# Kernel optimization log

Measured on AMD Instinct MI355X. Metric: run time of the kernel, lower is better.

## Reference

```python
import jax, jax.numpy as jnp
import numpy as np

B, D = 8192, 1024

def setup_inputs() -> dict:
    key = jax.random.key(0)
    ks = jax.random.split(key, 5)
    scale = 1.0 / np.sqrt(D)
    return {
        "x": jax.random.normal(ks[0], (B, D), dtype=jnp.float32),
        "h": jax.random.normal(ks[1], (B, D), dtype=jnp.float32),
        "c": jax.random.normal(ks[2], (B, D), dtype=jnp.float32),
        # gate order: [input, forget, output, candidate]
        "Wx": jax.random.normal(ks[3], (4, D, D), dtype=jnp.float32) * scale,
        "Wh": jax.random.normal(ks[4], (4, D, D), dtype=jnp.float32) * scale,
    }

def reference(x, h, c, Wx, Wh):
    # two batched GEMMs covering all 8 projections: [B,D] x [4,D,D] -> [4,B,D]
    gx = jnp.einsum('bd,gdk->gbk', x, Wx)
    gh = jnp.einsum('bd,gdk->gbk', h, Wh)
    g = gx + gh
    i = jax.nn.sigmoid(g[0])
    f = jax.nn.sigmoid(g[1])
    o = jax.nn.sigmoid(g[2])
    u = jnp.tanh(g[3])
    c_t = i * u + f * c
    h_t = o * jnp.tanh(c_t)
    return (h_t, c_t)
```

## Files before the change

kernel.cpp:

```cpp
#include <hip/hip_runtime.h>
#include <hip/hip_bf16.h>
#include <cstdint>


#define B_DIM 8192
#define D_DIM 1024
#define K_DIM 2048

typedef __attribute__((ext_vector_type(8))) short bf16x8;
typedef __attribute__((ext_vector_type(4))) float f32x4;
typedef __attribute__((ext_vector_type(4))) unsigned int u32x4;

static __device__ __forceinline__ unsigned short f2bf(float f) {
  union { float f; unsigned int u; } v; v.f = f;
  unsigned int u = v.u;
  unsigned int r = (u + 0x7FFFu + ((u >> 16) & 1u)) >> 16;
  return (unsigned short)r;
}

static __device__ __forceinline__ void load16(const void* gp, void* lp) {
  __builtin_amdgcn_global_load_lds(
      (const __attribute__((address_space(1))) void*)gp,
      (__attribute__((address_space(3))) void*)lp, 16, 0, 0);
}

static __device__ __forceinline__ float sigmoid_f(float x) {
  return 1.0f / (1.0f + __expf(-x));
}
static __device__ __forceinline__ float tanh_f(float x) {
  float e = __expf(-2.0f * fabsf(x));
  float r = (1.0f - e) / (1.0f + e);
  return copysignf(r, x);
}

__global__ __launch_bounds__(256) void pack_a_kernel(
    const float* __restrict__ x, const float* __restrict__ h,
    unsigned short* __restrict__ Apack) {
  int t = blockIdx.x * 256 + threadIdx.x;
  size_t base = (size_t)t * 8;
  int b = (int)(base >> 11);
  int k = (int)(base & 2047);
  const float* src = (k < 1024) ? (x + (size_t)b * 1024 + k)
                                : (h + (size_t)b * 1024 + (k - 1024));
  float4 v0 = ((const float4*)src)[0];
  float4 v1 = ((const float4*)src)[1];
  union { unsigned short s[8]; u32x4 v; } o;
  o.s[0] = f2bf(v0.x); o.s[1] = f2bf(v0.y); o.s[2] = f2bf(v0.z); o.s[3] = f2bf(v0.w);
  o.s[4] = f2bf(v1.x); o.s[5] = f2bf(v1.y); o.s[6] = f2bf(v1.z); o.s[7] = f2bf(v1.w);
  *(u32x4*)(Apack + base) = o.v;
}

__global__ __launch_bounds__(256) void prep_w_kernel(
    const float* __restrict__ Wx, const float* __restrict__ Wh,
    unsigned short* __restrict__ Wt) {
  __shared__ float tile[32][33];
  int bid = blockIdx.x;
  int g = bid >> 11;
  int rem = bid & 2047;
  int kt = rem >> 5;
  int nt = rem & 31;
  int k0 = kt * 32, n0 = nt * 32;
  int tx = threadIdx.x & 31, ty = threadIdx.x >> 5;
  const float* Wsrc;
  int ks;
  if (k0 < 1024) { Wsrc = Wx + (size_t)g * 1048576; ks = k0; }
  else           { Wsrc = Wh + (size_t)g * 1048576; ks = k0 - 1024; }
  #pragma unroll
  for (int s = 0; s < 4; ++s) {
    int r = ty + s * 8;
    tile[r][tx] = Wsrc[(size_t)(ks + r) * 1024 + n0 + tx];
  }
  __syncthreads();
  #pragma unroll
  for (int s = 0; s < 4; ++s) {
    int r = ty + s * 8;
    Wt[(size_t)((g << 10) + n0 + r) * 2048 + k0 + tx] = f2bf(tile[tx][r]);
  }
}

__global__ __launch_bounds__(256, 2) void lstm_gemm_kernel(
    const unsigned short* __restrict__ Apack,
    const unsigned short* __restrict__ Wt,
    const float* __restrict__ cprev,
    float* __restrict__ out) {
  extern __shared__ char lds[];
  const int tid = threadIdx.x;
  const int l = tid & 63;
  const int w = tid >> 6;
  const int bid = blockIdx.x;
  const int mt = bid >> 5;
  const int nt = bid & 31;
  const int m0 = mt << 7;
  const int n0 = nt << 5;

  f32x4 acc[4][2][2];
  #pragma unroll
  for (int g = 0; g < 4; ++g)
    #pragma unroll
    for (int a = 0; a < 2; ++a)
      #pragma unroll
      for (int b = 0; b < 2; ++b) acc[g][a][b] = (f32x4)0.0f;

  auto stage = [&](int buf, int t) {
    const int k0 = t << 6;
    char* base = lds + buf * 32768;
    #pragma unroll
    for (int j = 0; j < 4; ++j) {
      int c = j * 256 + tid;
      int Dd = c << 4;
      int row = Dd >> 7;
      int kbs = (Dd & 127) ^ ((row & 7) << 4);
      const unsigned short* gp = Apack + (size_t)(m0 + row) * 2048 + k0 + (kbs >> 1);
      load16(gp, base + ((c & ~63) << 4));
    }
    #pragma unroll
    for (int g = 0; g < 4; ++g) {
      int Dd = tid << 4;
      int row = Dd >> 7;
      int kbs = (Dd & 127) ^ ((row & 7) << 4);
      const unsigned short* gp =
          Wt + (size_t)((g << 10) + n0 + row) * 2048 + k0 + (kbs >> 1);
      load16(gp, base + 16384 + (g << 12) + ((tid & ~63) << 4));
    }
  };

  const int lr = l & 15;
  const int kgrp = (l >> 4) << 4;
  const int arow = w * 32 + lr;
  const int sA = (arow & 7) << 4;
  const int sB = (lr & 7) << 4;

  stage(0, 0);
  int cur = 0;
  for (int t = 0; t < 32; ++t) {
    __syncthreads();
    if (t + 1 < 32) stage(cur ^ 1, t + 1);
    const char* Ab = lds + cur * 32768;
    const char* Bb = Ab + 16384;
    #pragma unroll
    for (int ks = 0; ks < 2; ++ks) {
      const int kb = ks * 64 + kgrp;
      bf16x8 a0 = *(const bf16x8*)(Ab + arow * 128 + (kb ^ sA));
      bf16x8 a1 = *(const bf16x8*)(Ab + (arow + 16) * 128 + (kb ^ sA));
      #pragma unroll
      for (int g = 0; g < 4; ++g) {
        const char* Bg = Bb + (g << 12);
        bf16x8 b0 = *(const bf16x8*)(Bg + lr * 128 + (kb ^ sB));
        bf16x8 b1 = *(const bf16x8*)(Bg + (lr + 16) * 128 + (kb ^ sB));
        acc[g][0][0] = __builtin_amdgcn_mfma_f32_16x16x32_bf16(a0, b0, acc[g][0][0], 0, 0, 0);
        acc[g][0][1] = __builtin_amdgcn_mfma_f32_16x16x32_bf16(a0, b1, acc[g][0][1], 0, 0, 0);
        acc[g][1][0] = __builtin_amdgcn_mfma_f32_16x16x32_bf16(a1, b0, acc[g][1][0], 0, 0, 0);
        acc[g][1][1] = __builtin_amdgcn_mfma_f32_16x16x32_bf16(a1, b1, acc[g][1][1], 0, 0, 0);
      }
    }
    cur ^= 1;
  }

  const int rbase = m0 + w * 32;
  #pragma unroll
  for (int mf = 0; mf < 2; ++mf) {
    #pragma unroll
    for (int nf = 0; nf < 2; ++nf) {
      int col = n0 + nf * 16 + lr;
      #pragma unroll
      for (int j = 0; j < 4; ++j) {
        int rrow = rbase + mf * 16 + ((l >> 4) << 2) + j;
        float gi = acc[0][mf][nf][j];
        float gf = acc[1][mf][nf][j];
        float go = acc[2][mf][nf][j];
        float gu = acc[3][mf][nf][j];
        float i_ = sigmoid_f(gi);
        float f_ = sigmoid_f(gf);
        float o_ = sigmoid_f(go);
        float u_ = tanh_f(gu);
        size_t idx = (size_t)rrow * 1024 + col;
        float ct = i_ * u_ + f_ * cprev[idx];
        float ht = o_ * tanh_f(ct);
        out[idx] = ht;
        out[8388608 + idx] = ct;
      }
    }
  }
}

extern "C" void kernel_launch(void* const* d_in, const int* in_sizes, int n_in,
                              void* d_out, int out_size, void* d_ws, size_t ws_size,
                              hipStream_t stream) {
  const float* x  = (const float*)d_in[0];
  const float* h  = (const float*)d_in[1];
  const float* c  = (const float*)d_in[2];
  const float* Wx = (const float*)d_in[3];
  const float* Wh = (const float*)d_in[4];
  float* out = (float*)d_out;

  unsigned short* Apack = (unsigned short*)d_ws;
  unsigned short* Wt = (unsigned short*)((char*)d_ws + 33554432);

  pack_a_kernel<<<8192, 256, 0, stream>>>(x, h, Apack);
  prep_w_kernel<<<8192, 256, 0, stream>>>(Wx, Wh, Wt);
  lstm_gemm_kernel<<<2048, 256, 65536, stream>>>(Apack, Wt, c, out);
}
```

Baseline: 171.3 us.

## Enlarge GEMM tile to 128x64 with 8 waves and triple-buffered LDS pipeline

The fused LSTM GEMM now uses 512-thread blocks, each computing a 128-row by 64-column (times 4 gates) tile. Work is split over 8 waves in a 2x4 grid, and each wave holds 16 accumulator fragments, which gives more MFMA reuse per LDS load. The K loop switches from double buffering with a syncthreads per step to a three-slot ring that prefetches two stages ahead, using explicit vmcnt waits, raw barriers, sched_barrier fences and setprio around the MFMA bursts. The block needs 144 KB of dynamic LDS, set via hipFuncSetAttribute. That likely limits occupancy to one block per CU despite the launch-bounds hint, so latency hiding now rests on the deeper prefetch.

New measurement: 175.9 us. +2.7%, slower.

```diff
diff --git a/kernel.cpp b/kernel.cpp
--- a/kernel.cpp
+++ b/kernel.cpp
@@ -3,9 +3,8 @@
 #include <cstdint>
 
 
-#define B_DIM 8192
-#define D_DIM 1024
-#define K_DIM 2048
+#define LDS_SLOT  49152
+#define LDS_TOTAL 147456
 
 typedef __attribute__((ext_vector_type(8))) short bf16x8;
 typedef __attribute__((ext_vector_type(4))) float f32x4;
@@ -78,7 +77,7 @@
   }
 }
 
-__global__ __launch_bounds__(256, 2) void lstm_gemm_kernel(
+__global__ __launch_bounds__(512, 2) void lstm_gemm_kernel(
     const unsigned short* __restrict__ Apack,
     const unsigned short* __restrict__ Wt,
     const float* __restrict__ cprev,
@@ -87,26 +86,26 @@
   const int tid = threadIdx.x;
   const int l = tid & 63;
   const int w = tid >> 6;
+  const int wr = w >> 2;
+  const int wc = w & 3;
   const int bid = blockIdx.x;
-  const int mt = bid >> 5;
-  const int nt = bid & 31;
+  const int mt = bid >> 4;
+  const int nt = bid & 15;
   const int m0 = mt << 7;
-  const int n0 = nt << 5;
-
-  f32x4 acc[4][2][2];
-  #pragma unroll
-  for (int g = 0; g < 4; ++g)
-    #pragma unroll
-    for (int a = 0; a < 2; ++a)
-      #pragma unroll
-      for (int b = 0; b < 2; ++b) acc[g][a][b] = (f32x4)0.0f;
-
-  auto stage = [&](int buf, int t) {
+  const int n0 = nt << 6;
+
+  f32x4 acc[4][4];
+  #pragma unroll
+  for (int mf = 0; mf < 4; ++mf)
+    #pragma unroll
+    for (int g = 0; g < 4; ++g) acc[mf][g] = (f32x4)0.0f;
+
+  auto stage = [&](int slot, int t) {
     const int k0 = t << 6;
-    char* base = lds + buf * 32768;
-    #pragma unroll
-    for (int j = 0; j < 4; ++j) {
-      int c = j * 256 + tid;
+    char* base = lds + slot * LDS_SLOT;
+    #pragma unroll
+    for (int j = 0; j < 2; ++j) {
+      int c = j * 512 + tid;
       int Dd = c << 4;
       int row = Dd >> 7;
       int kbs = (Dd & 127) ^ ((row & 7) << 4);
@@ -120,65 +119,88 @@
       int kbs = (Dd & 127) ^ ((row & 7) << 4);
       const unsigned short* gp =
           Wt + (size_t)((g << 10) + n0 + row) * 2048 + k0 + (kbs >> 1);
-      load16(gp, base + 16384 + (g << 12) + ((tid & ~63) << 4));
+      load16(gp, base + 16384 + (g << 13) + ((tid & ~63) << 4));
     }
   };
 
   const int lr = l & 15;
   const int kgrp = (l >> 4) << 4;
-  const int arow = w * 32 + lr;
-  const int sA = (arow & 7) << 4;
-  const int sB = (lr & 7) << 4;
+  const int arow = wr * 64 + lr;
+  const int brow = wc * 16 + lr;
+  const int sxr = (lr & 7) << 4;
 
   stage(0, 0);
-  int cur = 0;
+  stage(1, 1);
+
+  int sc = 0;
+  #pragma unroll 1
   for (int t = 0; t < 32; ++t) {
-    __syncthreads();
-    if (t + 1 < 32) stage(cur ^ 1, t + 1);
-    const char* Ab = lds + cur * 32768;
+    if (t < 31) asm volatile("s_waitcnt vmcnt(6)" ::: "memory");
+    else        asm volatile("s_waitcnt vmcnt(0)" ::: "memory");
+    __builtin_amdgcn_sched_barrier(0);
+    __builtin_amdgcn_s_barrier();
+    __builtin_amdgcn_sched_barrier(0);
+    if (t + 2 < 32) {
+      int sn = sc + 2; if (sn >= 3) sn -= 3;
+      stage(sn, t + 2);
+    }
+    __builtin_amdgcn_sched_barrier(0);
+    const char* Ab = lds + sc * LDS_SLOT;
     const char* Bb = Ab + 16384;
     #pragma unroll
-    for (int ks = 0; ks < 2; ++ks) {
-      const int kb = ks * 64 + kgrp;
-      bf16x8 a0 = *(const bf16x8*)(Ab + arow * 128 + (kb ^ sA));
-      bf16x8 a1 = *(const bf16x8*)(Ab + (arow + 16) * 128 + (kb ^ sA));
-      #pragma unroll
-      for (int g = 0; g < 4; ++g) {
-        const char* Bg = Bb + (g << 12);
-        bf16x8 b0 = *(const bf16x8*)(Bg + lr * 128 + (kb ^ sB));
-        bf16x8 b1 = *(const bf16x8*)(Bg + (lr + 16) * 128 + (kb ^ sB));
-        acc[g][0][0] = __builtin_amdgcn_mfma_f32_16x16x32_bf16(a0, b0, acc[g][0][0], 0, 0, 0);
-        acc[g][0][1] = __builtin_amdgcn_mfma_f32_16x16x32_bf16(a0, b1, acc[g][0][1], 0, 0, 0);
-        acc[g][1][0] = __builtin_amdgcn_mfma_f32_16x16x32_bf16(a1, b0, acc[g][1][0], 0, 0, 0);
-        acc[g][1][1] = __builtin_amdgcn_mfma_f32_16x16x32_bf16(a1, b1, acc[g][1][1], 0, 0, 0);
-      }
-    }
-    cur ^= 1;
-  }
-
-  const int rbase = m0 + w * 32;
-  #pragma unroll
-  for (int mf = 0; mf < 2; ++mf) {
-    #pragma unroll
-    for (int nf = 0; nf < 2; ++nf) {
-      int col = n0 + nf * 16 + lr;
-      #pragma unroll
-      for (int j = 0; j < 4; ++j) {
-        int rrow = rbase + mf * 16 + ((l >> 4) << 2) + j;
-        float gi = acc[0][mf][nf][j];
-        float gf = acc[1][mf][nf][j];
-        float go = acc[2][mf][nf][j];
-        float gu = acc[3][mf][nf][j];
-        float i_ = sigmoid_f(gi);
-        float f_ = sigmoid_f(gf);
-        float o_ = sigmoid_f(go);
-        float u_ = tanh_f(gu);
-        size_t idx = (size_t)rrow * 1024 + col;
-        float ct = i_ * u_ + f_ * cprev[idx];
-        float ht = o_ * tanh_f(ct);
-        out[idx] = ht;
-        out[8388608 + idx] = ct;
-      }
+    for (int kk = 0; kk < 2; ++kk) {
+      const int kbs = (kk * 64 + kgrp) ^ sxr;
+      bf16x8 a0 = *(const bf16x8*)(Ab + (arow     ) * 128 + kbs);
+      bf16x8 a1 = *(const bf16x8*)(Ab + (arow + 16) * 128 + kbs);
+      bf16x8 a2 = *(const bf16x8*)(Ab + (arow + 32) * 128 + kbs);
+      bf16x8 a3 = *(const bf16x8*)(Ab + (arow + 48) * 128 + kbs);
+      bf16x8 b0 = *(const bf16x8*)(Bb +         brow * 128 + kbs);
+      bf16x8 b1 = *(const bf16x8*)(Bb +  8192 + brow * 128 + kbs);
+      bf16x8 b2 = *(const bf16x8*)(Bb + 16384 + brow * 128 + kbs);
+      bf16x8 b3 = *(const bf16x8*)(Bb + 24576 + brow * 128 + kbs);
+      __builtin_amdgcn_s_setprio(1);
+      acc[0][0] = __builtin_amdgcn_mfma_f32_16x16x32_bf16(a0, b0, acc[0][0], 0, 0, 0);
+      acc[0][1] = __builtin_amdgcn_mfma_f32_16x16x32_bf16(a0, b1, acc[0][1], 0, 0, 0);
+      acc[0][2] = __builtin_amdgcn_mfma_f32_16x16x32_bf16(a0, b2, acc[0][2], 0, 0, 0);
+      acc[0][3] = __builtin_amdgcn_mfma_f32_16x16x32_bf16(a0, b3, acc[0][3], 0, 0, 0);
+      acc[1][0] = __builtin_amdgcn_mfma_f32_16x16x32_bf16(a1, b0, acc[1][0], 0, 0, 0);
+      acc[1][1] = __builtin_amdgcn_mfma_f32_16x16x32_bf16(a1, b1, acc[1][1], 0, 0, 0);
+      acc[1][2] = __builtin_amdgcn_mfma_f32_16x16x32_bf16(a1, b2, acc[1][2], 0, 0, 0);
+      acc[1][3] = __builtin_amdgcn_mfma_f32_16x16x32_bf16(a1, b3, acc[1][3], 0, 0, 0);
+      acc[2][0] = __builtin_amdgcn_mfma_f32_16x16x32_bf16(a2, b0, acc[2][0], 0, 0, 0);
+      acc[2][1] = __builtin_amdgcn_mfma_f32_16x16x32_bf16(a2, b1, acc[2][1], 0, 0, 0);
+      acc[2][2] = __builtin_amdgcn_mfma_f32_16x16x32_bf16(a2, b2, acc[2][2], 0, 0, 0);
+      acc[2][3] = __builtin_amdgcn_mfma_f32_16x16x32_bf16(a2, b3, acc[2][3], 0, 0, 0);
+      acc[3][0] = __builtin_amdgcn_mfma_f32_16x16x32_bf16(a3, b0, acc[3][0], 0, 0, 0);
+      acc[3][1] = __builtin_amdgcn_mfma_f32_16x16x32_bf16(a3, b1, acc[3][1], 0, 0, 0);
+      acc[3][2] = __builtin_amdgcn_mfma_f32_16x16x32_bf16(a3, b2, acc[3][2], 0, 0, 0);
+      acc[3][3] = __builtin_amdgcn_mfma_f32_16x16x32_bf16(a3, b3, acc[3][3], 0, 0, 0);
+      __builtin_amdgcn_s_setprio(0);
+      __builtin_amdgcn_sched_barrier(0);
+    }
+    sc += 1; if (sc >= 3) sc -= 3;
+  }
+
+  const int q = (l >> 4) << 2;
+  const int col = n0 + wc * 16 + lr;
+  #pragma unroll
+  for (int mf = 0; mf < 4; ++mf) {
+    #pragma unroll
+    for (int j = 0; j < 4; ++j) {
+      int row = m0 + wr * 64 + mf * 16 + q + j;
+      float gi = acc[mf][0][j];
+      float gf = acc[mf][1][j];
+      float go = acc[mf][2][j];
+      float gu = acc[mf][3][j];
+      float i_ = sigmoid_f(gi);
+      float f_ = sigmoid_f(gf);
+      float o_ = sigmoid_f(go);
+      float u_ = tanh_f(gu);
+      size_t idx = (size_t)row * 1024 + col;
+      float ct = i_ * u_ + f_ * cprev[idx];
+      float ht = o_ * tanh_f(ct);
+      out[idx] = ht;
+      out[8388608 + idx] = ct;
     }
   }
 }
@@ -196,7 +218,10 @@
   unsigned short* Apack = (unsigned short*)d_ws;
   unsigned short* Wt = (unsigned short*)((char*)d_ws + 33554432);
 
+  hipFuncSetAttribute((const void*)lstm_gemm_kernel,
+                      hipFuncAttributeMaxDynamicSharedMemorySize, LDS_TOTAL);
+
   pack_a_kernel<<<8192, 256, 0, stream>>>(x, h, Apack);
   prep_w_kernel<<<8192, 256, 0, stream>>>(Wx, Wh, Wt);
-  lstm_gemm_kernel<<<2048, 256, 65536, stream>>>(Apack, Wt, c, out);
-}
+  lstm_gemm_kernel<<<dim3(1024), dim3(512), LDS_TOTAL, stream>>>(Apack, Wt, c, out);
+}
```

## Enlarge GEMM block tile to 256x64 with 2x2 wave grid and XCD-aware mapping

Applied to the files above, without the earlier changes.

Each block now computes a 256-row by 64-column tile across all four gates, using 128KB of double-buffered LDS. A 2x2 wave layout gives each wave 128x32 outputs with 64 accumulator fragments, and operand fragments are read into registers once per k-step. Block IDs are remapped so that column tiles are grouped per XCD for better L2 reuse of weights. This raises arithmetic intensity and cuts global/LDS traffic per FLOP, at the cost of one block per CU, heavy register pressure and fewer blocks in the grid.

Result: slower. 244.6 us (+42.8%).

```diff
diff --git a/kernel.cpp b/kernel.cpp
--- a/kernel.cpp
+++ b/kernel.cpp
@@ -3,9 +3,7 @@
 #include <cstdint>
 
 
-#define B_DIM 8192
-#define D_DIM 1024
-#define K_DIM 2048
+#define LDS_TOTAL 131072
 
 typedef __attribute__((ext_vector_type(8))) short bf16x8;
 typedef __attribute__((ext_vector_type(4))) float f32x4;
@@ -78,7 +76,7 @@
   }
 }
 
-__global__ __launch_bounds__(256, 2) void lstm_gemm_kernel(
+__global__ __launch_bounds__(256, 1) void lstm_gemm_kernel(
     const unsigned short* __restrict__ Apack,
     const unsigned short* __restrict__ Wt,
     const float* __restrict__ cprev,
@@ -87,93 +85,125 @@
   const int tid = threadIdx.x;
   const int l = tid & 63;
   const int w = tid >> 6;
-  const int bid = blockIdx.x;
-  const int mt = bid >> 5;
-  const int nt = bid & 31;
-  const int m0 = mt << 7;
-  const int n0 = nt << 5;
-
-  f32x4 acc[4][2][2];
-  #pragma unroll
-  for (int g = 0; g < 4; ++g)
-    #pragma unroll
-    for (int a = 0; a < 2; ++a)
-      #pragma unroll
-      for (int b = 0; b < 2; ++b) acc[g][a][b] = (f32x4)0.0f;
-
-  auto stage = [&](int buf, int t) {
-    const int k0 = t << 6;
-    char* base = lds + buf * 32768;
-    #pragma unroll
-    for (int j = 0; j < 4; ++j) {
-      int c = j * 256 + tid;
-      int Dd = c << 4;
-      int row = Dd >> 7;
-      int kbs = (Dd & 127) ^ ((row & 7) << 4);
-      const unsigned short* gp = Apack + (size_t)(m0 + row) * 2048 + k0 + (kbs >> 1);
-      load16(gp, base + ((c & ~63) << 4));
-    }
-    #pragma unroll
-    for (int g = 0; g < 4; ++g) {
-      int Dd = tid << 4;
-      int row = Dd >> 7;
-      int kbs = (Dd & 127) ^ ((row & 7) << 4);
-      const unsigned short* gp =
-          Wt + (size_t)((g << 10) + n0 + row) * 2048 + k0 + (kbs >> 1);
-      load16(gp, base + 16384 + (g << 12) + ((tid & ~63) << 4));
-    }
-  };
+  const int wr = w >> 1;
+  const int wc = w & 1;
+  const int bid0 = blockIdx.x;
+  const int xcd = bid0 & 7;
+  const int cc = bid0 >> 3;
+  const int nt = xcd * 2 + (cc >> 5);
+  const int mt = cc & 31;
+  const int m0 = mt << 8;
+  const int n0 = nt << 6;
+
+  char* const buf0 = lds;
+  char* const buf1 = lds + 65536;
+
+  f32x4 acc[8][4][2];
+  #pragma unroll
+  for (int mf = 0; mf < 8; ++mf)
+    #pragma unroll
+    for (int g = 0; g < 4; ++g)
+      #pragma unroll
+      for (int nf = 0; nf < 2; ++nf) acc[mf][g][nf] = (f32x4)0.0f;
 
   const int lr = l & 15;
   const int kgrp = (l >> 4) << 4;
-  const int arow = w * 32 + lr;
-  const int sA = (arow & 7) << 4;
-  const int sB = (lr & 7) << 4;
-
-  stage(0, 0);
-  int cur = 0;
+  const int sx = (lr & 7) << 4;
+  const int kx0 = kgrp ^ sx;
+  const int kx1 = (64 + kgrp) ^ sx;
+  const int aoff = (wr * 128 + lr) * 128;
+  const int boff = 32768 + (wc * 32 + lr) * 128;
+
+  const int arl = tid >> 3;
+  const int akb = ((tid << 4) & 127) ^ ((arl & 7) << 4);
+  const unsigned short* const gAbase =
+      Apack + (size_t)(m0 + arl) * 2048 + (akb >> 1);
+  const unsigned short* const gBbase =
+      Wt + (size_t)(n0 + arl) * 2048 + (akb >> 1);
+  const int dbase = (tid & ~63) << 4;
+
+  auto stageAB = [&](char* bufb, int t) {
+    const unsigned short* ga = gAbase + (t << 6);
+    #pragma unroll
+    for (int p = 0; p < 8; ++p)
+      load16(ga + (size_t)p * 65536, bufb + p * 4096 + dbase);
+    const unsigned short* gb = gBbase + (t << 6);
+    #pragma unroll
+    for (int p = 0; p < 8; ++p)
+      load16(gb + (size_t)(p >> 1) * 2097152 + (size_t)(p & 1) * 65536,
+             bufb + 32768 + p * 4096 + dbase);
+  };
+
+  bf16x8 aR0[8], aR1[8];
+  bf16x8 bR0[4][2], bR1[4][2];
+
+  auto readAll = [&](const char* bufc) {
+    #pragma unroll
+    for (int mf = 0; mf < 8; ++mf) {
+      const char* p = bufc + aoff + mf * 2048;
+      aR0[mf] = *(const bf16x8*)(p + kx0);
+      aR1[mf] = *(const bf16x8*)(p + kx1);
+    }
+    #pragma unroll
+    for (int g = 0; g < 4; ++g)
+      #pragma unroll
+      for (int nf = 0; nf < 2; ++nf) {
+        const char* p = bufc + boff + g * 8192 + nf * 2048;
+        bR0[g][nf] = *(const bf16x8*)(p + kx0);
+        bR1[g][nf] = *(const bf16x8*)(p + kx1);
+      }
+  };
+
+  auto mfmaAll = [&]() {
+    #pragma unroll
+    for (int mf = 0; mf < 8; ++mf)
+      #pragma unroll
+      for (int g = 0; g < 4; ++g)
+        #pragma unroll
+        for (int nf = 0; nf < 2; ++nf)
+          acc[mf][g][nf] = __builtin_amdgcn_mfma_f32_16x16x32_bf16(
+              aR0[mf], bR0[g][nf], acc[mf][g][nf], 0, 0, 0);
+    #pragma unroll
+    for (int mf = 0; mf < 8; ++mf)
+      #pragma unroll
+      for (int g = 0; g < 4; ++g)
+        #pragma unroll
+        for (int nf = 0; nf < 2; ++nf)
+          acc[mf][g][nf] = __builtin_amdgcn_mfma_f32_16x16x32_bf16(
+              aR1[mf], bR1[g][nf], acc[mf][g][nf], 0, 0, 0);
+  };
+
+  stageAB(buf0, 0);
+  __syncthreads();
+
+  #pragma unroll 1
   for (int t = 0; t < 32; ++t) {
+    char* bufc = (t & 1) ? buf1 : buf0;
+    char* bufn = (t & 1) ? buf0 : buf1;
+    if (t + 1 < 32) stageAB(bufn, t + 1);
+    readAll(bufc);
+    mfmaAll();
     __syncthreads();
-    if (t + 1 < 32) stage(cur ^ 1, t + 1);
-    const char* Ab = lds + cur * 32768;
-    const char* Bb = Ab + 16384;
-    #pragma unroll
-    for (int ks = 0; ks < 2; ++ks) {
-      const int kb = ks * 64 + kgrp;
-      bf16x8 a0 = *(const bf16x8*)(Ab + arow * 128 + (kb ^ sA));
-      bf16x8 a1 = *(const bf16x8*)(Ab + (arow + 16) * 128 + (kb ^ sA));
-      #pragma unroll
-      for (int g = 0; g < 4; ++g) {
-        const char* Bg = Bb + (g << 12);
-        bf16x8 b0 = *(const bf16x8*)(Bg + lr * 128 + (kb ^ sB));
-        bf16x8 b1 = *(const bf16x8*)(Bg + (lr + 16) * 128 + (kb ^ sB));
-        acc[g][0][0] = __builtin_amdgcn_mfma_f32_16x16x32_bf16(a0, b0, acc[g][0][0], 0, 0, 0);
-        acc[g][0][1] = __builtin_amdgcn_mfma_f32_16x16x32_bf16(a0, b1, acc[g][0][1], 0, 0, 0);
-        acc[g][1][0] = __builtin_amdgcn_mfma_f32_16x16x32_bf16(a1, b0, acc[g][1][0], 0, 0, 0);
-        acc[g][1][1] = __builtin_amdgcn_mfma_f32_16x16x32_bf16(a1, b1, acc[g][1][1], 0, 0, 0);
-      }
-    }
-    cur ^= 1;
-  }
-
-  const int rbase = m0 + w * 32;
-  #pragma unroll
-  for (int mf = 0; mf < 2; ++mf) {
+  }
+
+  const int q = (l >> 4) << 2;
+  #pragma unroll
+  for (int mf = 0; mf < 8; ++mf) {
     #pragma unroll
     for (int nf = 0; nf < 2; ++nf) {
-      int col = n0 + nf * 16 + lr;
+      const int col = n0 + wc * 32 + nf * 16 + lr;
       #pragma unroll
       for (int j = 0; j < 4; ++j) {
-        int rrow = rbase + mf * 16 + ((l >> 4) << 2) + j;
-        float gi = acc[0][mf][nf][j];
-        float gf = acc[1][mf][nf][j];
-        float go = acc[2][mf][nf][j];
-        float gu = acc[3][mf][nf][j];
+        int row = m0 + wr * 128 + mf * 16 + q + j;
+        float gi = acc[mf][0][nf][j];
+        float gf = acc[mf][1][nf][j];
+        float go = acc[mf][2][nf][j];
+        float gu = acc[mf][3][nf][j];
         float i_ = sigmoid_f(gi);
         float f_ = sigmoid_f(gf);
         float o_ = sigmoid_f(go);
         float u_ = tanh_f(gu);
-        size_t idx = (size_t)rrow * 1024 + col;
+        size_t idx = (size_t)row * 1024 + col;
         float ct = i_ * u_ + f_ * cprev[idx];
         float ht = o_ * tanh_f(ct);
         out[idx] = ht;
@@ -196,7 +226,10 @@
   unsigned short* Apack = (unsigned short*)d_ws;
   unsigned short* Wt = (unsigned short*)((char*)d_ws + 33554432);
 
+  hipFuncSetAttribute((const void*)lstm_gemm_kernel,
+                      hipFuncAttributeMaxDynamicSharedMemorySize, LDS_TOTAL);
+
   pack_a_kernel<<<8192, 256, 0, stream>>>(x, h, Apack);
   prep_w_kernel<<<8192, 256, 0, stream>>>(Wx, Wh, Wt);
-  lstm_gemm_kernel<<<2048, 256, 65536, stream>>>(Apack, Wt, c, out);
-}
+  lstm_gemm_kernel<<<dim3(512), dim3(256), LDS_TOTAL, stream>>>(Apack, Wt, c, out);
+}
```
